# Performance work log

Measured on AMD Instinct MI355X. Metric: run time of the kernel, lower is better.

## Reference

```python
import jax, jax.numpy as jnp
import numpy as np

N_ENT = 100000
D = 128
N_EDGES = 1600000
B = 8192
EPS = 1e-5


def setup_inputs() -> dict:
    key = jax.random.key(0)
    ks = jax.random.split(key, 12)
    return {
        "E": jax.random.normal(ks[0], (N_ENT, D), jnp.float32),
        "gamma": jnp.ones((D,), jnp.float32),
        "beta": jnp.zeros((D,), jnp.float32),
        "W_gnn": jax.random.normal(ks[1], (D, D), jnp.float32) / np.sqrt(D),
        "b_gnn": jnp.zeros((D,), jnp.float32),
        "W_g": jax.random.normal(ks[2], (D,), jnp.float32) / np.sqrt(D),
        "b_g": jnp.zeros((), jnp.float32),
        "W_age": jax.random.normal(ks[3], (D, 7), jnp.float32) / np.sqrt(D),
        "b_age": jnp.zeros((7,), jnp.float32),
        "W_occ": jax.random.normal(ks[4], (D, 21), jnp.float32) / np.sqrt(D),
        "b_occ": jnp.zeros((21,), jnp.float32),
        "src": jax.random.randint(ks[5], (N_EDGES,), 0, N_ENT, jnp.int32),
        "dst": jax.random.randint(ks[6], (N_EDGES,), 0, N_ENT, jnp.int32),
        "neighbor": jax.random.randint(ks[7], (B,), 0, N_ENT, jnp.int32),
        "gender": jax.random.randint(ks[8], (B,), 0, 2, jnp.int32),
        "age": jax.random.randint(ks[9], (B,), 0, 7, jnp.int32),
        "occupation": jax.random.randint(ks[10], (B,), 0, 21, jnp.int32),
    }


def reference(E, gamma, beta, W_gnn, b_gnn, W_g, b_g, W_age, b_age, W_occ, b_occ,
              src, dst, neighbor, gender, age, occupation):
    n = E.shape[0]
    # encoder (embedding of all nodes) -> batchnorm over node axis
    mu = jnp.mean(E, axis=0)
    var = jnp.var(E, axis=0)
    h = (E - mu) * jax.lax.rsqrt(var + EPS) * gamma + beta  # [N, D]
    # gnn: mean neighbor aggregation over edge list, then linear + relu
    agg = jax.ops.segment_sum(h[src], dst, num_segments=n)  # [N, D]
    deg = jax.ops.segment_sum(jnp.ones_like(src, jnp.float32), dst, num_segments=n)
    agg = agg / jnp.maximum(deg, 1.0)[:, None]
    h = jax.nn.relu(agg @ W_gnn + b_gnn)  # [N, D]
    # gather walked-to nodes; gradient-reversal layer is identity in forward
    u = h[neighbor]  # [B, D]
    gender_pred = u @ W_g + b_g            # [B]
    age_pred = u @ W_age + b_age           # [B, 7]
    occ_pred = u @ W_occ + b_occ           # [B, 21]
    # mode == 'gender': BCEWithLogitsLoss (mean)
    z = gender.astype(jnp.float32)
    x = gender_pred
    loss_adv = jnp.mean(jnp.maximum(x, 0.0) - x * z + jnp.log1p(jnp.exp(-jnp.abs(x))))
    return (loss_adv, age_pred, gender_pred, occ_pred)
```

## Files before the change

kernel.cpp:

```cpp
#include <hip/hip_runtime.h>
#include <math.h>

#define N_ENT   100000
#define DIM     128
#define N_EDGES 1600000
#define BATCH   8192
#define EPS     1e-5f
#define CAP     64
#define NSTAT_BLK 512
#define HW_LD   132
#define A_LD    132

#define WS_SCALE     256
#define WS_SHIFT     384
#define WS_BCOUNT    528
#define WS_SLOTOF    8720
#define WS_BUCKET    108720
#define WS_PARTIAL   633008
#define WS_EBF       764080

__device__ __forceinline__ unsigned bfpack(float a, float b) {
    unsigned ua = __float_as_uint(a);
    unsigned ub = __float_as_uint(b);
    ua = (ua + 0x7FFFu + ((ua >> 16) & 1u)) >> 16;
    ub = (ub + 0x7FFFu + ((ub >> 16) & 1u)) & 0xFFFF0000u;
    return ua | ub;
}
__device__ __forceinline__ float bflo(unsigned u) { return __uint_as_float(u << 16); }
__device__ __forceinline__ float bfhi(unsigned u) { return __uint_as_float(u & 0xFFFF0000u); }

__global__ __launch_bounds__(256) void stats_init_kernel(const float4* __restrict__ E4,
                                                         const int* __restrict__ neighbor,
                                                         int* __restrict__ slot_of,
                                                         int* __restrict__ bcount,
                                                         uint2* __restrict__ ebf2,
                                                         float* __restrict__ out_loss,
                                                         float* __restrict__ partial) {
    int t = threadIdx.x;
    if (blockIdx.x >= NSTAT_BLK) {
        int n = (blockIdx.x - NSTAT_BLK) * 256 + t;
        if (n < BATCH) {
            bcount[n] = 0;
            slot_of[neighbor[n]] = n;
        }
        if (n == 0) out_loss[0] = 0.f;
        return;
    }
    int sid = blockIdx.x;
    int cg = t & 31;
    int rs = t >> 5;
    const int STRIDE = NSTAT_BLK * 8;
    float sx = 0.f, sy = 0.f, sz = 0.f, sw = 0.f;
    float qx = 0.f, qy = 0.f, qz = 0.f, qw = 0.f;
    const float4 z4 = make_float4(0.f, 0.f, 0.f, 0.f);
    for (int r = sid * 8 + rs; r < N_ENT; r += 8 * STRIDE) {
        float4 v[8];
        int rr[8];
#pragma unroll
        for (int k = 0; k < 8; ++k) {
            rr[k] = r + k * STRIDE;
            v[k] = (rr[k] < N_ENT) ? E4[(size_t)rr[k] * 32 + cg] : z4;
        }
#pragma unroll
        for (int k = 0; k < 8; ++k) {
            if (rr[k] < N_ENT) {
                uint2 p;
                p.x = bfpack(v[k].x, v[k].y);
                p.y = bfpack(v[k].z, v[k].w);
                ebf2[(size_t)rr[k] * 32 + cg] = p;
            }
            sx += v[k].x; sy += v[k].y; sz += v[k].z; sw += v[k].w;
            qx += v[k].x * v[k].x; qy += v[k].y * v[k].y;
            qz += v[k].z * v[k].z; qw += v[k].w * v[k].w;
        }
    }
    __shared__ float sh[8 * 256];
    sh[0 * 256 + t] = sx; sh[1 * 256 + t] = sy;
    sh[2 * 256 + t] = sz; sh[3 * 256 + t] = sw;
    sh[4 * 256 + t] = qx; sh[5 * 256 + t] = qy;
    sh[6 * 256 + t] = qz; sh[7 * 256 + t] = qw;
    __syncthreads();
    for (int o = 128; o >= 32; o >>= 1) {
        if (t < o) {
#pragma unroll
            for (int j = 0; j < 8; ++j) sh[j * 256 + t] += sh[j * 256 + t + o];
        }
        __syncthreads();
    }
    if (t < 32) {
#pragma unroll
        for (int j = 0; j < 8; ++j)
            partial[sid * 256 + j * 32 + t] = sh[j * 256 + t];
    }
}

__global__ __launch_bounds__(256) void edge_finalize_kernel(const int4* __restrict__ src4,
                                                            const int4* __restrict__ dst4,
                                                            const int* __restrict__ slot_of,
                                                            int* __restrict__ bcount,
                                                            int* __restrict__ bucket,
                                                            const float* __restrict__ partial,
                                                            const float* __restrict__ gamma,
                                                            const float* __restrict__ beta,
                                                            float* __restrict__ scale,
                                                            float* __restrict__ shift) {
    if (blockIdx.x == 0) {
        int t = threadIdx.x;
        float s = 0.f;
#pragma unroll 16
        for (int b = 0; b < NSTAT_BLK; ++b) s += partial[b * 256 + t];
        __shared__ float tot[256];
        tot[t] = s;
        __syncthreads();
        if (t < 128) {
            int ti = t >> 2, j = t & 3;
            const float invn = 1.0f / (float)N_ENT;
            float mu = tot[j * 32 + ti] * invn;
            float var = tot[(j + 4) * 32 + ti] * invn - mu * mu;
            float rs = rsqrtf(var + EPS);
            float sc = gamma[t] * rs;
            scale[t] = sc;
            shift[t] = beta[t] - mu * sc;
        }
        return;
    }
    const int n4 = N_EDGES / 4;
    int tid = (blockIdx.x - 1) * blockDim.x + threadIdx.x;
    int e0 = tid * 2;
    int e1 = tid * 2 + 1;
    if (e0 >= n4) return;
    int4 d0 = dst4[e0];
    int4 s0 = src4[e0];
    bool has1 = (e1 < n4);
    int4 d1 = has1 ? dst4[e1] : make_int4(0, 0, 0, 0);
    int4 s1 = has1 ? src4[e1] : make_int4(0, 0, 0, 0);
    int sl0 = slot_of[d0.x];
    int sl1 = slot_of[d0.y];
    int sl2 = slot_of[d0.z];
    int sl3 = slot_of[d0.w];
    int sl4 = has1 ? slot_of[d1.x] : -1;
    int sl5 = has1 ? slot_of[d1.y] : -1;
    int sl6 = has1 ? slot_of[d1.z] : -1;
    int sl7 = has1 ? slot_of[d1.w] : -1;
    if (sl0 >= 0) { int p = atomicAdd(&bcount[sl0], 1); if (p < CAP) bucket[sl0 * CAP + p] = s0.x; }
    if (sl1 >= 0) { int p = atomicAdd(&bcount[sl1], 1); if (p < CAP) bucket[sl1 * CAP + p] = s0.y; }
    if (sl2 >= 0) { int p = atomicAdd(&bcount[sl2], 1); if (p < CAP) bucket[sl2 * CAP + p] = s0.z; }
    if (sl3 >= 0) { int p = atomicAdd(&bcount[sl3], 1); if (p < CAP) bucket[sl3 * CAP + p] = s0.w; }
    if (sl4 >= 0) { int p = atomicAdd(&bcount[sl4], 1); if (p < CAP) bucket[sl4 * CAP + p] = s1.x; }
    if (sl5 >= 0) { int p = atomicAdd(&bcount[sl5], 1); if (p < CAP) bucket[sl5 * CAP + p] = s1.y; }
    if (sl6 >= 0) { int p = atomicAdd(&bcount[sl6], 1); if (p < CAP) bucket[sl6 * CAP + p] = s1.z; }
    if (sl7 >= 0) { int p = atomicAdd(&bcount[sl7], 1); if (p < CAP) bucket[sl7 * CAP + p] = s1.w; }
}

__global__ __launch_bounds__(256) void item_fused_kernel(const uint4* __restrict__ ebf4,
                                                         const int* __restrict__ neighbor,
                                                         const int* __restrict__ gender,
                                                         const int* __restrict__ slot_of,
                                                         const int* __restrict__ bcount,
                                                         const int* __restrict__ bucket,
                                                         const float* __restrict__ scale,
                                                         const float* __restrict__ shift,
                                                         const float4* __restrict__ W4,
                                                         const float4* __restrict__ bias4,
                                                         const float* __restrict__ W_g,
                                                         const float* __restrict__ b_g,
                                                         const float* __restrict__ W_age,
                                                         const float* __restrict__ b_age,
                                                         const float* __restrict__ W_occ,
                                                         const float* __restrict__ b_occ,
                                                         float* __restrict__ out_age,
                                                         float* __restrict__ out_gender,
                                                         float* __restrict__ out_occ,
                                                         float* __restrict__ out_loss) {
    __shared__ __align__(16) float A_s[8 * A_LD];
    __shared__ __align__(16) float HW[29 * HW_LD];
    __shared__ float sh[256];
    __shared__ float hb[32];
    __shared__ int   cslot_s[8];
    const int t = threadIdx.x;
    const int item0 = blockIdx.x * 8;

    if (t < 8) cslot_s[t] = slot_of[neighbor[item0 + t]];
    for (int idx = t; idx < 29 * 128; idx += 256) {
        int h = idx >> 7;
        int d = idx & 127;
        float v;
        if (h < 7)       v = W_age[d * 7 + h];
        else if (h < 28) v = W_occ[d * 21 + (h - 7)];
        else             v = W_g[d];
        HW[h * HW_LD + d] = v;
    }
    if (t < 29) hb[t] = (t < 7) ? b_age[t] : (t < 28) ? b_occ[t - 7] : b_g[0];
    __syncthreads();

    {
        const int lane = t & 63;
        const int q  = lane & 15;
        const int es = (lane >> 4) & 1;
        const int li = t >> 5;
        int cs = cslot_s[li];
        int dg = bcount[cs];
        int m = dg < CAP ? dg : CAP;
        const int* bk = bucket + cs * CAP;
        float a0 = 0.f, a1 = 0.f, a2 = 0.f, a3 = 0.f;
        float a4 = 0.f, a5 = 0.f, a6 = 0.f, a7 = 0.f;
        int iters = (m + 15) >> 4;
        int mm1 = m > 0 ? m - 1 : 0;
        for (int it = 0; it < iters; ++it) {
            int e0 = it * 16 + es;
            int rr[8];
            unsigned ok[8];
#pragma unroll
            for (int j = 0; j < 8; ++j) {
                int e = e0 + 2 * j;
                int ec = e < mm1 ? e : mm1;
                rr[j] = bk[ec];
                ok[j] = (e < m) ? 0xFFFFFFFFu : 0u;
            }
            uint4 v[8];
#pragma unroll
            for (int j = 0; j < 8; ++j)
                v[j] = ebf4[(size_t)rr[j] * 16 + q];
#pragma unroll
            for (int j = 0; j < 8; ++j) {
                unsigned mk = ok[j];
                a0 += bflo(v[j].x & mk); a1 += bfhi(v[j].x & mk);
                a2 += bflo(v[j].y & mk); a3 += bfhi(v[j].y & mk);
                a4 += bflo(v[j].z & mk); a5 += bfhi(v[j].z & mk);
                a6 += bflo(v[j].w & mk); a7 += bfhi(v[j].w & mk);
            }
        }
        a0 += __shfl_down(a0, 16); a1 += __shfl_down(a1, 16);
        a2 += __shfl_down(a2, 16); a3 += __shfl_down(a3, 16);
        a4 += __shfl_down(a4, 16); a5 += __shfl_down(a5, 16);
        a6 += __shfl_down(a6, 16); a7 += __shfl_down(a7, 16);
        if (es == 0) {
            float4* dst = (float4*)(A_s + li * A_LD + q * 8);
            dst[0] = make_float4(a0, a1, a2, a3);
            dst[1] = make_float4(a4, a5, a6, a7);
        }
    }
    __syncthreads();

    const int row = t >> 5;
    const int c4  = t & 31;
    {
        int cs = cslot_s[row];
        float fdg = (float)bcount[cs];
        float rd = 1.0f / fmaxf(fdg, 1.0f);
        float4 v = ((float4*)(A_s + row * A_LD))[c4];
        float4 sc = ((const float4*)scale)[c4];
        float4 sf = ((const float4*)shift)[c4];
        float4 o;
        o.x = (v.x * sc.x + fdg * sf.x) * rd;
        o.y = (v.y * sc.y + fdg * sf.y) * rd;
        o.z = (v.z * sc.z + fdg * sf.z) * rd;
        o.w = (v.w * sc.w + fdg * sf.w) * rd;
        ((float4*)(A_s + row * A_LD))[c4] = o;
    }
    __syncthreads();

    {
        const int ks = t & 7;
        const int cg = t >> 3;
        float acc[8][4];
#pragma unroll
        for (int r = 0; r < 8; ++r) {
            acc[r][0] = 0.f; acc[r][1] = 0.f; acc[r][2] = 0.f; acc[r][3] = 0.f;
        }
#pragma unroll 4
        for (int kk = 0; kk < 16; ++kk) {
            int k = ks + 8 * kk;
            float4 wv = W4[k * 32 + cg];
#pragma unroll
            for (int r = 0; r < 8; ++r) {
                float a = A_s[r * A_LD + k];
                acc[r][0] += a * wv.x; acc[r][1] += a * wv.y;
                acc[r][2] += a * wv.z; acc[r][3] += a * wv.w;
            }
        }
#pragma unroll
        for (int off = 4; off > 0; off >>= 1) {
#pragma unroll
            for (int r = 0; r < 8; ++r) {
                acc[r][0] += __shfl_down(acc[r][0], off);
                acc[r][1] += __shfl_down(acc[r][1], off);
                acc[r][2] += __shfl_down(acc[r][2], off);
                acc[r][3] += __shfl_down(acc[r][3], off);
            }
        }
        float4 bv = bias4[cg];
        __syncthreads();
        if (ks == 0) {
#pragma unroll
            for (int r = 0; r < 8; ++r) {
                float4 o2;
                o2.x = fmaxf(acc[r][0] + bv.x, 0.f);
                o2.y = fmaxf(acc[r][1] + bv.y, 0.f);
                o2.z = fmaxf(acc[r][2] + bv.z, 0.f);
                o2.w = fmaxf(acc[r][3] + bv.w, 0.f);
                ((float4*)(A_s + r * A_LD))[cg] = o2;
            }
        }
    }
    __syncthreads();

    float val = 0.f;
    if (c4 < 29) {
        const float4* h4 = (const float4*)(A_s + row * A_LD);
        const float4* w4 = (const float4*)(HW + c4 * HW_LD);
        float b0 = hb[c4], b1 = 0.f, b2 = 0.f, b3 = 0.f;
#pragma unroll 8
        for (int dd = 0; dd < 32; ++dd) {
            float4 hv = h4[dd];
            float4 wv = w4[dd];
            b0 += hv.x * wv.x;
            b1 += hv.y * wv.y;
            b2 += hv.z * wv.z;
            b3 += hv.w * wv.w;
        }
        float x = b0 + b1 + b2 + b3;
        int item = item0 + row;
        if (c4 < 7)       out_age[item * 7 + c4] = x;
        else if (c4 < 28) out_occ[item * 21 + (c4 - 7)] = x;
        else {
            out_gender[item] = x;
            float z = (float)gender[item];
            val = fmaxf(x, 0.f) - x * z + log1pf(expf(-fabsf(x)));
        }
    }
    sh[t] = val;
    __syncthreads();
    for (int o = 128; o > 0; o >>= 1) {
        if (t < o) sh[t] += sh[t + o];
        __syncthreads();
    }
    if (t == 0) atomicAdd(out_loss, sh[0] * (1.0f / (float)BATCH));
}

extern "C" void kernel_launch(void* const* d_in, const int* in_sizes, int n_in,
                              void* d_out, int out_size, void* d_ws, size_t ws_size,
                              hipStream_t stream) {
    const float* E      = (const float*)d_in[0];
    const float* gamma  = (const float*)d_in[1];
    const float* beta   = (const float*)d_in[2];
    const float* W_gnn  = (const float*)d_in[3];
    const float* b_gnn  = (const float*)d_in[4];
    const float* W_g    = (const float*)d_in[5];
    const float* b_g    = (const float*)d_in[6];
    const float* W_age  = (const float*)d_in[7];
    const float* b_age  = (const float*)d_in[8];
    const float* W_occ  = (const float*)d_in[9];
    const float* b_occ  = (const float*)d_in[10];
    const int*   src    = (const int*)d_in[11];
    const int*   dst    = (const int*)d_in[12];
    const int*   neigh  = (const int*)d_in[13];
    const int*   gender = (const int*)d_in[14];

    float* ws  = (float*)d_ws;
    int*   wsi = (int*)d_ws;
    float* scale   = ws + WS_SCALE;
    float* shift   = ws + WS_SHIFT;
    int*   bcount  = wsi + WS_BCOUNT;
    int*   slot_of = wsi + WS_SLOTOF;
    int*   bucket  = wsi + WS_BUCKET;
    float* partial = ws + WS_PARTIAL;
    unsigned* ebf  = (unsigned*)(wsi + WS_EBF);

    float* out       = (float*)d_out;
    float* out_loss  = out;
    float* out_age   = out + 1;
    float* out_gen   = out + 1 + BATCH * 7;
    float* out_occ   = out + 1 + BATCH * 7 + BATCH;

    stats_init_kernel<<<NSTAT_BLK + BATCH / 256, 256, 0, stream>>>(
        (const float4*)E, neigh, slot_of, bcount, (uint2*)ebf, out_loss, partial);
    {
        const int n4 = N_EDGES / 4;
        int nthreads = (n4 + 1) / 2;
        int eblocks = (nthreads + 255) / 256;
        edge_finalize_kernel<<<1 + eblocks, 256, 0, stream>>>(
            (const int4*)src, (const int4*)dst, slot_of, bcount, bucket,
            partial, gamma, beta, scale, shift);
    }
    item_fused_kernel<<<BATCH / 8, 256, 0, stream>>>(
        (const uint4*)ebf, neigh, gender, slot_of, bcount, bucket, scale, shift,
        (const float4*)W_gnn, (const float4*)b_gnn,
        W_g, b_g, W_age, b_age, W_occ, b_occ,
        out_age, out_gen, out_occ, out_loss);
}
```

Baseline: 187.0 us.

## Overlap stats pass with edge bucketing and widen item kernel to 512 threads

Splits the slot-map initialization into its own small kernel so that the batchnorm statistics pass over E and the edge bucketing pass can run as one launch, in different blocks, letting the two memory-bound phases overlap. Finalization of scale and shift moves into a separate single-block kernel. The item kernel goes to 512 threads, using one wavefront per item for the neighbor gather with jmax-guarded loads and a split GEMV row assignment, which adds parallelism and outstanding memory requests per item. The trade-off is an extra kernel launch and a different register and occupancy profile for the item kernel.

```diff
diff --git a/kernel.cpp b/kernel.cpp
--- a/kernel.cpp
+++ b/kernel.cpp
@@ -8,6 +8,7 @@
 #define EPS     1e-5f
 #define CAP     64
 #define NSTAT_BLK 512
+#define NEDGE_BLK 782
 #define HW_LD   132
 #define A_LD    132
 
@@ -29,21 +30,54 @@
 __device__ __forceinline__ float bflo(unsigned u) { return __uint_as_float(u << 16); }
 __device__ __forceinline__ float bfhi(unsigned u) { return __uint_as_float(u & 0xFFFF0000u); }
 
-__global__ __launch_bounds__(256) void stats_init_kernel(const float4* __restrict__ E4,
-                                                         const int* __restrict__ neighbor,
-                                                         int* __restrict__ slot_of,
-                                                         int* __restrict__ bcount,
-                                                         uint2* __restrict__ ebf2,
-                                                         float* __restrict__ out_loss,
-                                                         float* __restrict__ partial) {
+__global__ __launch_bounds__(256) void init_kernel(const int* __restrict__ neighbor,
+                                                   int* __restrict__ slot_of,
+                                                   int* __restrict__ bcount,
+                                                   float* __restrict__ out_loss) {
+    int n = blockIdx.x * 256 + threadIdx.x;
+    if (n < BATCH) {
+        bcount[n] = 0;
+        slot_of[neighbor[n]] = n;
+    }
+    if (n == 0) out_loss[0] = 0.f;
+}
+
+__global__ __launch_bounds__(256) void stats_edges_kernel(const float4* __restrict__ E4,
+                                                          const int4* __restrict__ src4,
+                                                          const int4* __restrict__ dst4,
+                                                          const int* __restrict__ slot_of,
+                                                          int* __restrict__ bcount,
+                                                          int* __restrict__ bucket,
+                                                          uint2* __restrict__ ebf2,
+                                                          float* __restrict__ partial) {
     int t = threadIdx.x;
     if (blockIdx.x >= NSTAT_BLK) {
-        int n = (blockIdx.x - NSTAT_BLK) * 256 + t;
-        if (n < BATCH) {
-            bcount[n] = 0;
-            slot_of[neighbor[n]] = n;
-        }
-        if (n == 0) out_loss[0] = 0.f;
+        const int n4 = N_EDGES / 4;
+        int tid = (blockIdx.x - NSTAT_BLK) * 256 + t;
+        int e0 = tid * 2;
+        if (e0 >= n4) return;
+        int e1 = e0 + 1;
+        int4 d0 = dst4[e0];
+        int4 s0 = src4[e0];
+        bool has1 = (e1 < n4);
+        int4 d1 = has1 ? dst4[e1] : make_int4(0, 0, 0, 0);
+        int4 s1 = has1 ? src4[e1] : make_int4(0, 0, 0, 0);
+        int sl0 = slot_of[d0.x];
+        int sl1 = slot_of[d0.y];
+        int sl2 = slot_of[d0.z];
+        int sl3 = slot_of[d0.w];
+        int sl4 = has1 ? slot_of[d1.x] : -1;
+        int sl5 = has1 ? slot_of[d1.y] : -1;
+        int sl6 = has1 ? slot_of[d1.z] : -1;
+        int sl7 = has1 ? slot_of[d1.w] : -1;
+        if (sl0 >= 0) { int p = atomicAdd(&bcount[sl0], 1); if (p < CAP) bucket[sl0 * CAP + p] = s0.x; }
+        if (sl1 >= 0) { int p = atomicAdd(&bcount[sl1], 1); if (p < CAP) bucket[sl1 * CAP + p] = s0.y; }
+        if (sl2 >= 0) { int p = atomicAdd(&bcount[sl2], 1); if (p < CAP) bucket[sl2 * CAP + p] = s0.z; }
+        if (sl3 >= 0) { int p = atomicAdd(&bcount[sl3], 1); if (p < CAP) bucket[sl3 * CAP + p] = s0.w; }
+        if (sl4 >= 0) { int p = atomicAdd(&bcount[sl4], 1); if (p < CAP) bucket[sl4 * CAP + p] = s1.x; }
+        if (sl5 >= 0) { int p = atomicAdd(&bcount[sl5], 1); if (p < CAP) bucket[sl5 * CAP + p] = s1.y; }
+        if (sl6 >= 0) { int p = atomicAdd(&bcount[sl6], 1); if (p < CAP) bucket[sl6 * CAP + p] = s1.z; }
+        if (sl7 >= 0) { int p = atomicAdd(&bcount[sl7], 1); if (p < CAP) bucket[sl7 * CAP + p] = s1.w; }
         return;
     }
     int sid = blockIdx.x;
@@ -94,94 +128,60 @@
     }
 }
 
-__global__ __launch_bounds__(256) void edge_finalize_kernel(const int4* __restrict__ src4,
-                                                            const int4* __restrict__ dst4,
+__global__ __launch_bounds__(256) void finalize_kernel(const float* __restrict__ partial,
+                                                       const float* __restrict__ gamma,
+                                                       const float* __restrict__ beta,
+                                                       float* __restrict__ scale,
+                                                       float* __restrict__ shift) {
+    int t = threadIdx.x;
+    float s = 0.f;
+#pragma unroll 16
+    for (int b = 0; b < NSTAT_BLK; ++b) s += partial[b * 256 + t];
+    __shared__ float tot[256];
+    tot[t] = s;
+    __syncthreads();
+    if (t < 128) {
+        int ti = t >> 2, j = t & 3;
+        const float invn = 1.0f / (float)N_ENT;
+        float mu = tot[j * 32 + ti] * invn;
+        float var = tot[(j + 4) * 32 + ti] * invn - mu * mu;
+        float rs = rsqrtf(var + EPS);
+        float sc = gamma[t] * rs;
+        scale[t] = sc;
+        shift[t] = beta[t] - mu * sc;
+    }
+}
+
+__global__ __launch_bounds__(512, 8) void item_fused_kernel(const uint4* __restrict__ ebf4,
+                                                            const int* __restrict__ neighbor,
+                                                            const int* __restrict__ gender,
                                                             const int* __restrict__ slot_of,
-                                                            int* __restrict__ bcount,
-                                                            int* __restrict__ bucket,
-                                                            const float* __restrict__ partial,
-                                                            const float* __restrict__ gamma,
-                                                            const float* __restrict__ beta,
-                                                            float* __restrict__ scale,
-                                                            float* __restrict__ shift) {
-    if (blockIdx.x == 0) {
-        int t = threadIdx.x;
-        float s = 0.f;
-#pragma unroll 16
-        for (int b = 0; b < NSTAT_BLK; ++b) s += partial[b * 256 + t];
-        __shared__ float tot[256];
-        tot[t] = s;
-        __syncthreads();
-        if (t < 128) {
-            int ti = t >> 2, j = t & 3;
-            const float invn = 1.0f / (float)N_ENT;
-            float mu = tot[j * 32 + ti] * invn;
-            float var = tot[(j + 4) * 32 + ti] * invn - mu * mu;
-            float rs = rsqrtf(var + EPS);
-            float sc = gamma[t] * rs;
-            scale[t] = sc;
-            shift[t] = beta[t] - mu * sc;
-        }
-        return;
-    }
-    const int n4 = N_EDGES / 4;
-    int tid = (blockIdx.x - 1) * blockDim.x + threadIdx.x;
-    int e0 = tid * 2;
-    int e1 = tid * 2 + 1;
-    if (e0 >= n4) return;
-    int4 d0 = dst4[e0];
-    int4 s0 = src4[e0];
-    bool has1 = (e1 < n4);
-    int4 d1 = has1 ? dst4[e1] : make_int4(0, 0, 0, 0);
-    int4 s1 = has1 ? src4[e1] : make_int4(0, 0, 0, 0);
-    int sl0 = slot_of[d0.x];
-    int sl1 = slot_of[d0.y];
-    int sl2 = slot_of[d0.z];
-    int sl3 = slot_of[d0.w];
-    int sl4 = has1 ? slot_of[d1.x] : -1;
-    int sl5 = has1 ? slot_of[d1.y] : -1;
-    int sl6 = has1 ? slot_of[d1.z] : -1;
-    int sl7 = has1 ? slot_of[d1.w] : -1;
-    if (sl0 >= 0) { int p = atomicAdd(&bcount[sl0], 1); if (p < CAP) bucket[sl0 * CAP + p] = s0.x; }
-    if (sl1 >= 0) { int p = atomicAdd(&bcount[sl1], 1); if (p < CAP) bucket[sl1 * CAP + p] = s0.y; }
-    if (sl2 >= 0) { int p = atomicAdd(&bcount[sl2], 1); if (p < CAP) bucket[sl2 * CAP + p] = s0.z; }
-    if (sl3 >= 0) { int p = atomicAdd(&bcount[sl3], 1); if (p < CAP) bucket[sl3 * CAP + p] = s0.w; }
-    if (sl4 >= 0) { int p = atomicAdd(&bcount[sl4], 1); if (p < CAP) bucket[sl4 * CAP + p] = s1.x; }
-    if (sl5 >= 0) { int p = atomicAdd(&bcount[sl5], 1); if (p < CAP) bucket[sl5 * CAP + p] = s1.y; }
-    if (sl6 >= 0) { int p = atomicAdd(&bcount[sl6], 1); if (p < CAP) bucket[sl6 * CAP + p] = s1.z; }
-    if (sl7 >= 0) { int p = atomicAdd(&bcount[sl7], 1); if (p < CAP) bucket[sl7 * CAP + p] = s1.w; }
-}
-
-__global__ __launch_bounds__(256) void item_fused_kernel(const uint4* __restrict__ ebf4,
-                                                         const int* __restrict__ neighbor,
-                                                         const int* __restrict__ gender,
-                                                         const int* __restrict__ slot_of,
-                                                         const int* __restrict__ bcount,
-                                                         const int* __restrict__ bucket,
-                                                         const float* __restrict__ scale,
-                                                         const float* __restrict__ shift,
-                                                         const float4* __restrict__ W4,
-                                                         const float4* __restrict__ bias4,
-                                                         const float* __restrict__ W_g,
-                                                         const float* __restrict__ b_g,
-                                                         const float* __restrict__ W_age,
-                                                         const float* __restrict__ b_age,
-                                                         const float* __restrict__ W_occ,
-                                                         const float* __restrict__ b_occ,
-                                                         float* __restrict__ out_age,
-                                                         float* __restrict__ out_gender,
-                                                         float* __restrict__ out_occ,
-                                                         float* __restrict__ out_loss) {
+                                                            const int* __restrict__ bcount,
+                                                            const int* __restrict__ bucket,
+                                                            const float* __restrict__ scale,
+                                                            const float* __restrict__ shift,
+                                                            const float4* __restrict__ W4,
+                                                            const float4* __restrict__ bias4,
+                                                            const float* __restrict__ W_g,
+                                                            const float* __restrict__ b_g,
+                                                            const float* __restrict__ W_age,
+                                                            const float* __restrict__ b_age,
+                                                            const float* __restrict__ W_occ,
+                                                            const float* __restrict__ b_occ,
+                                                            float* __restrict__ out_age,
+                                                            float* __restrict__ out_gender,
+                                                            float* __restrict__ out_occ,
+                                                            float* __restrict__ out_loss) {
     __shared__ __align__(16) float A_s[8 * A_LD];
     __shared__ __align__(16) float HW[29 * HW_LD];
-    __shared__ float sh[256];
+    __shared__ float sh[512];
     __shared__ float hb[32];
     __shared__ int   cslot_s[8];
     const int t = threadIdx.x;
     const int item0 = blockIdx.x * 8;
 
     if (t < 8) cslot_s[t] = slot_of[neighbor[item0 + t]];
-    for (int idx = t; idx < 29 * 128; idx += 256) {
+    for (int idx = t; idx < 29 * 128; idx += 512) {
         int h = idx >> 7;
         int d = idx & 127;
         float v;
@@ -194,57 +194,67 @@
     __syncthreads();
 
     {
+        const int li   = t >> 6;
         const int lane = t & 63;
         const int q  = lane & 15;
-        const int es = (lane >> 4) & 1;
-        const int li = t >> 5;
+        const int es = lane >> 4;
         int cs = cslot_s[li];
         int dg = bcount[cs];
         int m = dg < CAP ? dg : CAP;
         const int* bk = bucket + cs * CAP;
         float a0 = 0.f, a1 = 0.f, a2 = 0.f, a3 = 0.f;
         float a4 = 0.f, a5 = 0.f, a6 = 0.f, a7 = 0.f;
-        int iters = (m + 15) >> 4;
+        int iters = (m + 31) >> 5;
         int mm1 = m > 0 ? m - 1 : 0;
         for (int it = 0; it < iters; ++it) {
-            int e0 = it * 16 + es;
+            int base = it * 32;
+            int rem = m - base;
+            int jmax = rem >= 32 ? 8 : ((rem + 3) >> 2);
             int rr[8];
             unsigned ok[8];
 #pragma unroll
             for (int j = 0; j < 8; ++j) {
-                int e = e0 + 2 * j;
-                int ec = e < mm1 ? e : mm1;
-                rr[j] = bk[ec];
-                ok[j] = (e < m) ? 0xFFFFFFFFu : 0u;
+                if (j < jmax) {
+                    int e = base + es + 4 * j;
+                    int ec = e < mm1 ? e : mm1;
+                    rr[j] = bk[ec];
+                    ok[j] = (e < m) ? 0xFFFFFFFFu : 0u;
+                }
             }
             uint4 v[8];
 #pragma unroll
             for (int j = 0; j < 8; ++j)
-                v[j] = ebf4[(size_t)rr[j] * 16 + q];
+                if (j < jmax) v[j] = ebf4[(size_t)rr[j] * 16 + q];
 #pragma unroll
             for (int j = 0; j < 8; ++j) {
-                unsigned mk = ok[j];
-                a0 += bflo(v[j].x & mk); a1 += bfhi(v[j].x & mk);
-                a2 += bflo(v[j].y & mk); a3 += bfhi(v[j].y & mk);
-                a4 += bflo(v[j].z & mk); a5 += bfhi(v[j].z & mk);
-                a6 += bflo(v[j].w & mk); a7 += bfhi(v[j].w & mk);
-            }
-        }
-        a0 += __shfl_down(a0, 16); a1 += __shfl_down(a1, 16);
-        a2 += __shfl_down(a2, 16); a3 += __shfl_down(a3, 16);
-        a4 += __shfl_down(a4, 16); a5 += __shfl_down(a5, 16);
-        a6 += __shfl_down(a6, 16); a7 += __shfl_down(a7, 16);
-        if (es == 0) {
-            float4* dst = (float4*)(A_s + li * A_LD + q * 8);
-            dst[0] = make_float4(a0, a1, a2, a3);
-            dst[1] = make_float4(a4, a5, a6, a7);
-        }
-    }
-    __syncthreads();
-
-    const int row = t >> 5;
-    const int c4  = t & 31;
-    {
+                if (j < jmax) {
+                    unsigned mk = ok[j];
+                    a0 += bflo(v[j].x & mk); a1 += bfhi(v[j].x & mk);
+                    a2 += bflo(v[j].y & mk); a3 += bfhi(v[j].y & mk);
+                    a4 += bflo(v[j].z & mk); a5 += bfhi(v[j].z & mk);
+                    a6 += bflo(v[j].w & mk); a7 += bfhi(v[j].w & mk);
+                }
+            }
+        }
+        a0 += __shfl_xor(a0, 16); a1 += __shfl_xor(a1, 16);
+        a2 += __shfl_xor(a2, 16); a3 += __shfl_xor(a3, 16);
+        a4 += __shfl_xor(a4, 16); a5 += __shfl_xor(a5, 16);
+        a6 += __shfl_xor(a6, 16); a7 += __shfl_xor(a7, 16);
+        a0 += __shfl_xor(a0, 32); a1 += __shfl_xor(a1, 32);
+        a2 += __shfl_xor(a2, 32); a3 += __shfl_xor(a3, 32);
+        a4 += __shfl_xor(a4, 32); a5 += __shfl_xor(a5, 32);
+        a6 += __shfl_xor(a6, 32); a7 += __shfl_xor(a7, 32);
+        if (lane < 32) {
+            float* dst = A_s + li * A_LD + q * 8;
+            if (es == 0) *(float4*)dst       = make_float4(a0, a1, a2, a3);
+            else         *(float4*)(dst + 4) = make_float4(a4, a5, a6, a7);
+        }
+    }
+    __syncthreads();
+
+    if (t < 256) {
+        int row = t >> 5;
+        int c4  = t & 31;
         int cs = cslot_s[row];
         float fdg = (float)bcount[cs];
         float rd = 1.0f / fmaxf(fdg, 1.0f);
@@ -262,10 +272,12 @@
 
     {
         const int ks = t & 7;
-        const int cg = t >> 3;
-        float acc[8][4];
-#pragma unroll
-        for (int r = 0; r < 8; ++r) {
+        const int rh = (t >> 3) & 1;
+        const int cg = t >> 4;
+        const int r0 = rh * 4;
+        float acc[4][4];
+#pragma unroll
+        for (int r = 0; r < 4; ++r) {
             acc[r][0] = 0.f; acc[r][1] = 0.f; acc[r][2] = 0.f; acc[r][3] = 0.f;
         }
 #pragma unroll 4
@@ -273,8 +285,8 @@
             int k = ks + 8 * kk;
             float4 wv = W4[k * 32 + cg];
 #pragma unroll
-            for (int r = 0; r < 8; ++r) {
-                float a = A_s[r * A_LD + k];
+            for (int r = 0; r < 4; ++r) {
+                float a = A_s[(r0 + r) * A_LD + k];
                 acc[r][0] += a * wv.x; acc[r][1] += a * wv.y;
                 acc[r][2] += a * wv.z; acc[r][3] += a * wv.w;
             }
@@ -282,7 +294,7 @@
 #pragma unroll
         for (int off = 4; off > 0; off >>= 1) {
 #pragma unroll
-            for (int r = 0; r < 8; ++r) {
+            for (int r = 0; r < 4; ++r) {
                 acc[r][0] += __shfl_down(acc[r][0], off);
                 acc[r][1] += __shfl_down(acc[r][1], off);
                 acc[r][2] += __shfl_down(acc[r][2], off);
@@ -293,45 +305,49 @@
         __syncthreads();
         if (ks == 0) {
 #pragma unroll
-            for (int r = 0; r < 8; ++r) {
+            for (int r = 0; r < 4; ++r) {
                 float4 o2;
                 o2.x = fmaxf(acc[r][0] + bv.x, 0.f);
                 o2.y = fmaxf(acc[r][1] + bv.y, 0.f);
                 o2.z = fmaxf(acc[r][2] + bv.z, 0.f);
                 o2.w = fmaxf(acc[r][3] + bv.w, 0.f);
-                ((float4*)(A_s + r * A_LD))[cg] = o2;
+                ((float4*)(A_s + (r0 + r) * A_LD))[cg] = o2;
             }
         }
     }
     __syncthreads();
 
     float val = 0.f;
-    if (c4 < 29) {
-        const float4* h4 = (const float4*)(A_s + row * A_LD);
-        const float4* w4 = (const float4*)(HW + c4 * HW_LD);
-        float b0 = hb[c4], b1 = 0.f, b2 = 0.f, b3 = 0.f;
+    if (t < 256) {
+        int row = t >> 5;
+        int h   = t & 31;
+        if (h < 29) {
+            const float4* h4 = (const float4*)(A_s + row * A_LD);
+            const float4* w4 = (const float4*)(HW + h * HW_LD);
+            float b0 = hb[h], b1 = 0.f, b2 = 0.f, b3 = 0.f;
 #pragma unroll 8
-        for (int dd = 0; dd < 32; ++dd) {
-            float4 hv = h4[dd];
-            float4 wv = w4[dd];
-            b0 += hv.x * wv.x;
-            b1 += hv.y * wv.y;
-            b2 += hv.z * wv.z;
-            b3 += hv.w * wv.w;
-        }
-        float x = b0 + b1 + b2 + b3;
-        int item = item0 + row;
-        if (c4 < 7)       out_age[item * 7 + c4] = x;
-        else if (c4 < 28) out_occ[item * 21 + (c4 - 7)] = x;
-        else {
-            out_gender[item] = x;
-            float z = (float)gender[item];
-            val = fmaxf(x, 0.f) - x * z + log1pf(expf(-fabsf(x)));
+            for (int dd = 0; dd < 32; ++dd) {
+                float4 hv = h4[dd];
+                float4 wv = w4[dd];
+                b0 += hv.x * wv.x;
+                b1 += hv.y * wv.y;
+                b2 += hv.z * wv.z;
+                b3 += hv.w * wv.w;
+            }
+            float x = b0 + b1 + b2 + b3;
+            int item = item0 + row;
+            if (h < 7)       out_age[item * 7 + h] = x;
+            else if (h < 28) out_occ[item * 21 + (h - 7)] = x;
+            else {
+                out_gender[item] = x;
+                float z = (float)gender[item];
+                val = fmaxf(x, 0.f) - x * z + log1pf(expf(-fabsf(x)));
+            }
         }
     }
     sh[t] = val;
     __syncthreads();
-    for (int o = 128; o > 0; o >>= 1) {
+    for (int o = 256; o > 0; o >>= 1) {
         if (t < o) sh[t] += sh[t + o];
         __syncthreads();
     }
@@ -373,17 +389,12 @@
     float* out_gen   = out + 1 + BATCH * 7;
     float* out_occ   = out + 1 + BATCH * 7 + BATCH;
 
-    stats_init_kernel<<<NSTAT_BLK + BATCH / 256, 256, 0, stream>>>(
-        (const float4*)E, neigh, slot_of, bcount, (uint2*)ebf, out_loss, partial);
-    {
-        const int n4 = N_EDGES / 4;
-        int nthreads = (n4 + 1) / 2;
-        int eblocks = (nthreads + 255) / 256;
-        edge_finalize_kernel<<<1 + eblocks, 256, 0, stream>>>(
-            (const int4*)src, (const int4*)dst, slot_of, bcount, bucket,
-            partial, gamma, beta, scale, shift);
-    }
-    item_fused_kernel<<<BATCH / 8, 256, 0, stream>>>(
+    init_kernel<<<BATCH / 256, 256, 0, stream>>>(neigh, slot_of, bcount, out_loss);
+    stats_edges_kernel<<<NSTAT_BLK + NEDGE_BLK, 256, 0, stream>>>(
+        (const float4*)E, (const int4*)src, (const int4*)dst,
+        slot_of, bcount, bucket, (uint2*)ebf, partial);
+    finalize_kernel<<<1, 256, 0, stream>>>(partial, gamma, beta, scale, shift);
+    item_fused_kernel<<<BATCH / 8, 512, 0, stream>>>(
         (const uint4*)ebf, neigh, gender, slot_of, bcount, bucket, scale, shift,
         (const float4*)W_gnn, (const float4*)b_gnn,
         W_g, b_g, W_age, b_age, W_occ, b_occ,
```

Result: slower. 221.0 us (+18.2%).
